# Kernel tuning notes

Hardware: AMD Instinct MI355X
Metric: run time of the kernel (lower is better)

Reference implementation:

```python
import jax, jax.numpy as jnp
import numpy as np

B = 4096          # effective_batch_size (world_size=1)
D = 128           # embedding_dim
T = 0.5           # temperature
CW = 0.5          # confidence_weight
PT = 0.8          # positive_threshold (cosine)


def setup_inputs() -> dict:
    key = jax.random.key(0)
    emb = jax.random.normal(key, (B, D), dtype=jnp.float32)
    emb = emb / jnp.linalg.norm(emb, axis=1, keepdims=True)  # cosine-sim embeddings
    return {"embedding": emb}


def reference(embedding):
    b = embedding.shape[0]
    half = b // 2
    idx = jnp.arange(b)
    pos_idx = (idx + half) % b  # positive pair index (other augmented view)

    # exp(sim / T), [B, B]
    sim = jnp.exp(embedding @ embedding.T / T)

    # precomputed masks (world_size=1, rank=0, num_pos=2):
    # positive mask: the other view; negative mask: everything except self and its pair
    pos_mask = jnp.zeros((b, b), dtype=sim.dtype).at[idx, pos_idx].set(1.0)
    neg_mask = 1.0 - pos_mask - jnp.eye(b, dtype=sim.dtype)

    all_pos = sim * pos_mask
    all_neg = sim * neg_mask

    pos_sim = sim[idx, pos_idx]  # [B]

    # diff_sim: |sim - pos_sim| on upper triangle (j >= i), 3 elsewhere,
    # with diagonal and (i, i+half) for i < half also set to 3
    upper = idx[None, :] >= idx[:, None]
    excl = jnp.eye(b, dtype=bool) | ((idx[:, None] < half) & (idx[None, :] == idx[:, None] + half))
    diff_sim = jnp.where(upper & ~excl, jnp.abs(sim - pos_sim[:, None]), jnp.asarray(3.0, sim.dtype))

    # all argmin locations (torch.where(diff_sim == min)) -> boolean select mask
    min_mask = diff_sim == jnp.min(diff_sim)
    conf = (jnp.log(pos_sim) * T >= PT)[:, None]  # per-anchor confidence gate
    sel = min_mask & conf

    # false-negative reweighting (pos read of all_neg happens before neg update)
    new_pos = jnp.where(sel & (all_pos == 0.0), CW * all_neg, all_pos)
    new_neg = jnp.where(sel & (all_neg != 0.0), (1.0 - CW) * all_neg, all_neg)

    pos = jnp.sum(new_pos, axis=1)
    neg = jnp.sum(new_neg, axis=1)
    return -jnp.mean(jnp.log(pos / (pos + neg)))
```

## Files before the change

### kernel.cpp

```cpp
#include <hip/hip_runtime.h>
#include <hip/hip_bf16.h>
#include <math.h>

#define B_N  4096
#define HALF 2048
#define D_K  128
#define TI   128
#define TJ   64
#define NTI  32
#define NTJ  64
#define JPB  4
#define NJG  (NTJ / JPB)

typedef __attribute__((ext_vector_type(8))) short bf16x8;
typedef __attribute__((ext_vector_type(4))) float f32x4;

__device__ __forceinline__ ushort f2bf(float x) {
    unsigned u = __float_as_uint(x);
    unsigned r = u + 0x7FFFu + ((u >> 16) & 1u);
    return (ushort)(r >> 16);
}

__device__ __forceinline__ void gload_lds16(const ushort* g, ushort* l) {
    __builtin_amdgcn_global_load_lds(
        (const __attribute__((address_space(1))) unsigned int*)g,
        (__attribute__((address_space(3))) unsigned int*)l, 16, 0, 0);
}

__device__ __forceinline__ bf16x8 read_fragB(const ushort* lds, int row, int kbyte) {
    int byte = ((row << 8) | kbyte) ^ ((row & 7) << 4);
    return *(const bf16x8*)((const char*)lds + byte);
}

__global__ __launch_bounds__(256) void k0_prep(const float* __restrict__ emb,
                                               ushort* __restrict__ embh,
                                               float* __restrict__ pos_sim,
                                               float* __restrict__ conf,
                                               float* __restrict__ neg_acc,
                                               unsigned* __restrict__ counter) {
    int gtid = blockIdx.x * 256 + threadIdx.x;
    float4 v = ((const float4*)emb)[gtid];
    float4 p = ((const float4*)emb)[gtid ^ 65536];
    ushort4 h;
    h.x = f2bf(v.x); h.y = f2bf(v.y); h.z = f2bf(v.z); h.w = f2bf(v.w);
    ((ushort4*)embh)[gtid] = h;
    float d = 0.f;
    d = fmaf(v.x, p.x, d); d = fmaf(v.y, p.y, d);
    d = fmaf(v.z, p.z, d); d = fmaf(v.w, p.w, d);
#pragma unroll
    for (int off = 1; off < 32; off <<= 1) d += __shfl_xor(d, off);
    if ((gtid & 31) == 0) {
        int r = gtid >> 5;
        float ps = expf(d * 2.0f);
        pos_sim[r] = ps;
        conf[r]    = (logf(ps) * 0.5f >= 0.8f) ? 1.0f : 0.0f;
        neg_acc[r] = 0.f;
    }
    if (gtid == 0) *counter = 0u;
}

__global__ __launch_bounds__(256, 3) void k1_main(const ushort* __restrict__ embh,
                                                  const float* __restrict__ pos_sim,
                                                  const float* __restrict__ conf,
                                                  float* __restrict__ neg_acc,
                                                  float* __restrict__ corrpart,
                                                  unsigned* __restrict__ tile_min) {
    int bi = blockIdx.y, jg = blockIdx.x;
    __shared__ ushort B0[TJ * D_K];
    __shared__ ushort B1[TJ * D_K];

    int tid = threadIdx.x, lane = tid & 63, wr = tid >> 6;
    int l15 = lane & 15;
    int k8  = (lane >> 4) << 3;
    int jr4 = (lane >> 4) << 2;

    {
        const ushort* srcB = embh + (size_t)(jg * JPB) * TJ * D_K;
#pragma unroll
        for (int it = 0; it < 4; ++it) {
            int f = tid + 256 * it;
            int r = f >> 4, c = f & 15;
            int g = (r << 4) | (c ^ (r & 7));
            gload_lds16(srcB + g * 8, B0 + f * 8);
        }
    }

    int I0 = bi * TI + wr * 32;
    bf16x8 A0[4], A1[4];
    {
        const ushort* a0 = embh + (size_t)(I0 + l15) * D_K + k8;
        const ushort* a1 = embh + (size_t)(I0 + 16 + l15) * D_K + k8;
#pragma unroll
        for (int ks = 0; ks < 4; ++ks) {
            A0[ks] = *(const bf16x8*)(a0 + ks * 32);
            A1[ks] = *(const bf16x8*)(a1 + ks * 32);
        }
    }

    int jtd = I0 >> 6;
    float psi0 = pos_sim[I0 + l15];
    float psi1 = pos_sim[I0 + 16 + l15];
    float cf0  = conf[I0 + l15];
    float cf1  = conf[I0 + 16 + l15];
    bool anyc  = __any((cf0 != 0.f) || (cf1 != 0.f));
    float negacc0 = 0.f, negacc1 = 0.f;
    float tl[JPB];

    __syncthreads();

#pragma unroll
    for (int t = 0; t < JPB; ++t) {
        const ushort* Bc = (t & 1) ? B1 : B0;
        ushort*       Bn = (t & 1) ? B0 : B1;
        int jt = jg * JPB + t;

        if (t + 1 < JPB) {
            const ushort* srcB = embh + (size_t)(jt + 1) * TJ * D_K;
#pragma unroll
            for (int it = 0; it < 4; ++it) {
                int f = tid + 256 * it;
                int r = f >> 4, c = f & 15;
                int g = (r << 4) | (c ^ (r & 7));
                gload_lds16(srcB + g * 8, Bn + f * 8);
            }
        }

        f32x4 acc[2][4];
#pragma unroll
        for (int m = 0; m < 2; ++m)
#pragma unroll
            for (int n = 0; n < 4; ++n) acc[m][n] = (f32x4){0.f, 0.f, 0.f, 0.f};
#pragma unroll
        for (int ks = 0; ks < 4; ++ks) {
            int kb = ks * 64 + (k8 << 1);
            bf16x8 b[4];
#pragma unroll
            for (int n = 0; n < 4; ++n) b[n] = read_fragB(Bc, l15 + n * 16, kb);
#pragma unroll
            for (int n = 0; n < 4; ++n) {
                acc[0][n] = __builtin_amdgcn_mfma_f32_16x16x32_bf16(b[n], A0[ks], acc[0][n], 0, 0, 0);
                acc[1][n] = __builtin_amdgcn_mfma_f32_16x16x32_bf16(b[n], A1[ks], acc[1][n], 0, 0, 0);
            }
        }
#pragma unroll
        for (int m = 0; m < 2; ++m)
#pragma unroll
            for (int n = 0; n < 4; ++n)
#pragma unroll
                for (int reg = 0; reg < 4; ++reg)
                    acc[m][n][reg] = __expf(acc[m][n][reg] * 2.0f);

        int j0 = jt * TJ;
        bool mixed = (jt == jtd), postt = (jt == (jtd ^ 32)), upT = (jt > jtd);
        float tmin = 3.0f;
#pragma unroll
        for (int m = 0; m < 2; ++m) {
            int i = I0 + m * 16 + l15;
            float psi = m ? psi1 : psi0;
            float np = 0.f;
            if (mixed) {
#pragma unroll
                for (int n = 0; n < 4; ++n)
#pragma unroll
                    for (int reg = 0; reg < 4; ++reg) {
                        float s = acc[m][n][reg];
                        int j = j0 + n * 16 + jr4 + reg;
                        if (j != i) np += s;
                        if (j > i)  tmin = fminf(tmin, fabsf(s - psi));
                    }
            } else if (postt) {
                int pidx = i ^ HALF;
#pragma unroll
                for (int n = 0; n < 4; ++n)
#pragma unroll
                    for (int reg = 0; reg < 4; ++reg) {
                        float s = acc[m][n][reg];
                        int j = j0 + n * 16 + jr4 + reg;
                        if (j != pidx) {
                            np += s;
                            if (upT) tmin = fminf(tmin, fabsf(s - psi));
                        }
                    }
            } else {
                float l0 = 3.f, l1 = 3.f, l2 = 3.f, l3 = 3.f;
#pragma unroll
                for (int n = 0; n < 4; ++n) {
                    float s0 = acc[m][n][0], s1 = acc[m][n][1];
                    float s2 = acc[m][n][2], s3 = acc[m][n][3];
                    np += (s0 + s1) + (s2 + s3);
                    if (upT) {
                        l0 = fminf(l0, fabsf(s0 - psi)); l1 = fminf(l1, fabsf(s1 - psi));
                        l2 = fminf(l2, fabsf(s2 - psi)); l3 = fminf(l3, fabsf(s3 - psi));
                    }
                }
                tmin = fminf(tmin, fminf(fminf(l0, l1), fminf(l2, l3)));
            }
            if (m) negacc1 += np; else negacc0 += np;
        }
        tl[t] = tmin;

        if (anyc) {
            float wt = tmin;
#pragma unroll
            for (int off = 32; off; off >>= 1)
                wt = fminf(wt, __shfl_xor(wt, off));
            tl[t] = wt;
#pragma unroll
            for (int m = 0; m < 2; ++m) {
                int i = I0 + m * 16 + l15;
                float psi = m ? psi1 : psi0;
                bool ci = ((m ? cf1 : cf0) != 0.f);
                float corr = 0.f;
#pragma unroll
                for (int n = 0; n < 4; ++n)
#pragma unroll
                    for (int reg = 0; reg < 4; ++reg) {
                        float s = acc[m][n][reg];
                        int j = j0 + n * 16 + jr4 + reg;
                        float d = 3.0f;
                        if (mixed)      { if (j > i) d = fabsf(s - psi); }
                        else if (postt) { if (upT && j != (i ^ HALF)) d = fabsf(s - psi); }
                        else if (upT)   d = fabsf(s - psi);
                        if (ci && d == wt) corr += 0.5f * s;
                    }
                corr += __shfl_xor(corr, 16);
                corr += __shfl_xor(corr, 32);
                if (lane < 16) corrpart[(size_t)jt * B_N + i] = corr;
            }
        }
        if (t + 1 < JPB) __syncthreads();
    }

#pragma unroll
    for (int off = 32; off; off >>= 1) {
#pragma unroll
        for (int t = 0; t < JPB; ++t)
            tl[t] = fminf(tl[t], __shfl_xor(tl[t], off));
    }
    if (lane == 0) {
        int base = (bi * 4 + wr) * NTJ + jg * JPB;
        tile_min[base + 0] = __float_as_uint(tl[0]);
        tile_min[base + 1] = __float_as_uint(tl[1]);
        tile_min[base + 2] = __float_as_uint(tl[2]);
        tile_min[base + 3] = __float_as_uint(tl[3]);
    }

    if (!anyc && lane < 16) {
#pragma unroll
        for (int t = 0; t < JPB; ++t) {
            corrpart[(size_t)(jg * JPB + t) * B_N + I0 + lane]      = 0.f;
            corrpart[(size_t)(jg * JPB + t) * B_N + I0 + 16 + lane] = 0.f;
        }
    }

    negacc0 += __shfl_xor(negacc0, 16);
    negacc0 += __shfl_xor(negacc0, 32);
    negacc1 += __shfl_xor(negacc1, 16);
    negacc1 += __shfl_xor(negacc1, 32);
    if (lane < 16) {
        atomicAdd(&neg_acc[I0 + lane],      negacc0);
        atomicAdd(&neg_acc[I0 + 16 + lane], negacc1);
    }
}

__global__ __launch_bounds__(128) void k3_loss(const float* __restrict__ pos_sim,
                                               const float* __restrict__ neg_acc,
                                               const float* __restrict__ corrpart,
                                               const unsigned* __restrict__ tile_min,
                                               float* __restrict__ partial,
                                               unsigned* __restrict__ counter,
                                               float* __restrict__ out) {
    int t = threadIdx.x, bi = blockIdx.x;
    unsigned gmv = 0xFFFFFFFFu;
#pragma unroll
    for (int k = 0; k < 64; ++k) gmv = min(gmv, tile_min[t + 128 * k]);
#pragma unroll
    for (int off = 32; off; off >>= 1) {
        unsigned o = (unsigned)__shfl_xor((int)gmv, off);
        gmv = min(gmv, o);
    }
    __shared__ unsigned gred[2];
    if ((t & 63) == 0) gred[t >> 6] = gmv;
    __syncthreads();
    unsigned gm = min(gred[0], gred[1]);

    int i = bi * 128 + t;
    int si = i >> 5;
    float corr = 0.f;
#pragma unroll 8
    for (int jt = 0; jt < NTJ; ++jt)
        if (tile_min[si * NTJ + jt] == gm)
            corr += corrpart[(size_t)jt * B_N + i];
    float pos = pos_sim[i] + corr;
    float neg = neg_acc[i] - corr;
    float l = logf(pos / (pos + neg));
#pragma unroll
    for (int off = 32; off; off >>= 1) l += __shfl_xor(l, off);
    __shared__ float w2[2];
    if ((t & 63) == 0) w2[t >> 6] = l;
    __syncthreads();
    if (t == 0) {
        partial[bi] = w2[0] + w2[1];
        __threadfence();
        unsigned c = atomicAdd(counter, 1u);
        if (c == NTI - 1) {
            __threadfence();
            float tot = 0.f;
            volatile float* vp = partial;
            for (int b = 0; b < NTI; ++b) tot += vp[b];
            *out = -tot / (float)B_N;
        }
    }
}

extern "C" void kernel_launch(void* const* d_in, const int* in_sizes, int n_in,
                              void* d_out, int out_size, void* d_ws, size_t ws_size,
                              hipStream_t stream) {
    const float* emb = (const float*)d_in[0];
    float* out = (float*)d_out;

    char* ws = (char*)d_ws;
    ushort*   embh      = (ushort*)ws;
    float*    fbase     = (float*)(ws + 1048576);
    float*    pos_sim   = fbase;
    float*    conf      = fbase + 4096;
    float*    neg_acc   = fbase + 8192;
    float*    corrpart  = fbase + 12288;
    float*    partial   = corrpart + (size_t)NTJ * B_N;
    unsigned* tile_min  = (unsigned*)(partial + 32);
    unsigned* counter   = tile_min + 128 * NTJ;

    k0_prep<<<512, 256, 0, stream>>>(emb, embh, pos_sim, conf, neg_acc, counter);
    k1_main<<<dim3(NJG, NTI), 256, 0, stream>>>(embh, pos_sim, conf, neg_acc,
                                                corrpart, tile_min);
    k3_loss<<<NTI, 128, 0, stream>>>(pos_sim, neg_acc, corrpart, tile_min,
                                     partial, counter, out);
}
```

Measured before the change: 32.62 us.

## Fuse loss reduction into main kernel via last-block-done tail

Removes the separate loss kernel. The last block of the main kernel, found with an atomic counter, now computes the global min, the corrections and the final mean. Per-row negative sums are written as 16 partial slices instead of atomically added, which also drops the zeroing in prep. The cost is that one block does the whole 4096-row tail serially, using a compacted list of min-matching tiles with a fallback path.

```diff
diff --git a/kernel.cpp b/kernel.cpp
--- a/kernel.cpp
+++ b/kernel.cpp
@@ -10,7 +10,8 @@
 #define NTI  32
 #define NTJ  64
 #define JPB  4
-#define NJG  (NTJ / JPB)
+#define NJG  16
+#define GRID 512
 
 typedef __attribute__((ext_vector_type(8))) short bf16x8;
 typedef __attribute__((ext_vector_type(4))) float f32x4;
@@ -36,8 +37,7 @@
                                                ushort* __restrict__ embh,
                                                float* __restrict__ pos_sim,
                                                float* __restrict__ conf,
-                                               float* __restrict__ neg_acc,
-                                               unsigned* __restrict__ counter) {
+                                               unsigned* __restrict__ fincnt) {
     int gtid = blockIdx.x * 256 + threadIdx.x;
     float4 v = ((const float4*)emb)[gtid];
     float4 p = ((const float4*)emb)[gtid ^ 65536];
@@ -54,25 +54,26 @@
         float ps = expf(d * 2.0f);
         pos_sim[r] = ps;
         conf[r]    = (logf(ps) * 0.5f >= 0.8f) ? 1.0f : 0.0f;
-        neg_acc[r] = 0.f;
-    }
-    if (gtid == 0) *counter = 0u;
+    }
+    if (gtid == 0) *fincnt = 0u;
 }
 
 __global__ __launch_bounds__(256, 3) void k1_main(const ushort* __restrict__ embh,
                                                   const float* __restrict__ pos_sim,
                                                   const float* __restrict__ conf,
-                                                  float* __restrict__ neg_acc,
+                                                  float* __restrict__ negpart,
                                                   float* __restrict__ corrpart,
-                                                  unsigned* __restrict__ tile_min) {
-    int bi = blockIdx.y, jg = blockIdx.x;
-    __shared__ ushort B0[TJ * D_K];
-    __shared__ ushort B1[TJ * D_K];
-
+                                                  unsigned* __restrict__ tile_min,
+                                                  unsigned* __restrict__ fincnt,
+                                                  float* __restrict__ out) {
     int tid = threadIdx.x, lane = tid & 63, wr = tid >> 6;
+    int bi = blockIdx.x >> 4, jg = blockIdx.x & 15;
     int l15 = lane & 15;
     int k8  = (lane >> 4) << 3;
     int jr4 = (lane >> 4) << 2;
+
+    __shared__ ushort B0[TJ * D_K];
+    __shared__ ushort B1[TJ * D_K];
 
     {
         const ushort* srcB = embh + (size_t)(jg * JPB) * TJ * D_K;
@@ -244,7 +245,6 @@
         tile_min[base + 2] = __float_as_uint(tl[2]);
         tile_min[base + 3] = __float_as_uint(tl[3]);
     }
-
     if (!anyc && lane < 16) {
 #pragma unroll
         for (int t = 0; t < JPB; ++t) {
@@ -252,65 +252,80 @@
             corrpart[(size_t)(jg * JPB + t) * B_N + I0 + 16 + lane] = 0.f;
         }
     }
-
     negacc0 += __shfl_xor(negacc0, 16);
     negacc0 += __shfl_xor(negacc0, 32);
     negacc1 += __shfl_xor(negacc1, 16);
     negacc1 += __shfl_xor(negacc1, 32);
     if (lane < 16) {
-        atomicAdd(&neg_acc[I0 + lane],      negacc0);
-        atomicAdd(&neg_acc[I0 + 16 + lane], negacc1);
-    }
-}
-
-__global__ __launch_bounds__(128) void k3_loss(const float* __restrict__ pos_sim,
-                                               const float* __restrict__ neg_acc,
-                                               const float* __restrict__ corrpart,
-                                               const unsigned* __restrict__ tile_min,
-                                               float* __restrict__ partial,
-                                               unsigned* __restrict__ counter,
-                                               float* __restrict__ out) {
-    int t = threadIdx.x, bi = blockIdx.x;
+        negpart[(size_t)jg * B_N + I0 + lane]      = negacc0;
+        negpart[(size_t)jg * B_N + I0 + 16 + lane] = negacc1;
+    }
+
+    __threadfence();
+    __syncthreads();
+    __shared__ unsigned rank;
+    if (tid == 0) rank = atomicAdd(fincnt, 1u);
+    __syncthreads();
+    if (rank != GRID - 1) return;
+    __threadfence();
+
+    __shared__ unsigned lcnt, gred[4], lslot[128];
+    __shared__ float w4[4];
+    if (tid == 0) lcnt = 0;
     unsigned gmv = 0xFFFFFFFFu;
 #pragma unroll
-    for (int k = 0; k < 64; ++k) gmv = min(gmv, tile_min[t + 128 * k]);
+    for (int k = 0; k < 32; ++k) gmv = min(gmv, tile_min[tid + 256 * k]);
 #pragma unroll
     for (int off = 32; off; off >>= 1) {
         unsigned o = (unsigned)__shfl_xor((int)gmv, off);
         gmv = min(gmv, o);
     }
-    __shared__ unsigned gred[2];
-    if ((t & 63) == 0) gred[t >> 6] = gmv;
-    __syncthreads();
-    unsigned gm = min(gred[0], gred[1]);
-
-    int i = bi * 128 + t;
-    int si = i >> 5;
-    float corr = 0.f;
-#pragma unroll 8
-    for (int jt = 0; jt < NTJ; ++jt)
-        if (tile_min[si * NTJ + jt] == gm)
-            corr += corrpart[(size_t)jt * B_N + i];
-    float pos = pos_sim[i] + corr;
-    float neg = neg_acc[i] - corr;
-    float l = logf(pos / (pos + neg));
-#pragma unroll
-    for (int off = 32; off; off >>= 1) l += __shfl_xor(l, off);
-    __shared__ float w2[2];
-    if ((t & 63) == 0) w2[t >> 6] = l;
-    __syncthreads();
-    if (t == 0) {
-        partial[bi] = w2[0] + w2[1];
-        __threadfence();
-        unsigned c = atomicAdd(counter, 1u);
-        if (c == NTI - 1) {
-            __threadfence();
-            float tot = 0.f;
-            volatile float* vp = partial;
-            for (int b = 0; b < NTI; ++b) tot += vp[b];
-            *out = -tot / (float)B_N;
-        }
-    }
+    if (lane == 0) gred[wr] = gmv;
+    __syncthreads();
+    unsigned gm = min(min(gred[0], gred[1]), min(gred[2], gred[3]));
+
+#pragma unroll
+    for (int k = 0; k < 32; ++k) {
+        int x = tid + 256 * k;
+        if (tile_min[x] == gm) {
+            unsigned p = atomicAdd(&lcnt, 1u);
+            if (p < 128) lslot[p] = (unsigned)x;
+        }
+    }
+    __syncthreads();
+    unsigned nl = lcnt;
+    bool fallback = (nl > 128u);
+    if (fallback) nl = 0;
+
+    float lsum = 0.f;
+#pragma unroll
+    for (int rr = 0; rr < 16; ++rr) {
+        int i = tid + rr * 256;
+        int si = i >> 5;
+        float nsum = 0.f;
+#pragma unroll
+        for (int p = 0; p < 16; ++p) nsum += negpart[(size_t)p * B_N + i];
+        float corr = 0.f;
+        if (!fallback) {
+            for (unsigned e = 0; e < nl; ++e) {
+                unsigned x = lslot[e];
+                if ((int)(x >> 6) == si) corr += corrpart[(size_t)(x & 63) * B_N + i];
+            }
+        } else {
+            for (int jt = 0; jt < NTJ; ++jt)
+                if (tile_min[si * NTJ + jt] == gm)
+                    corr += corrpart[(size_t)jt * B_N + i];
+        }
+        float pos = pos_sim[i] + corr;
+        float neg = nsum - corr;
+        lsum += logf(pos / (pos + neg));
+    }
+#pragma unroll
+    for (int off = 32; off; off >>= 1) lsum += __shfl_xor(lsum, off);
+    if (lane == 0) w4[wr] = lsum;
+    __syncthreads();
+    if (tid == 0)
+        *out = -((w4[0] + w4[1]) + (w4[2] + w4[3])) / (float)B_N;
 }
 
 extern "C" void kernel_launch(void* const* d_in, const int* in_sizes, int n_in,
@@ -320,19 +335,16 @@
     float* out = (float*)d_out;
 
     char* ws = (char*)d_ws;
-    ushort*   embh      = (ushort*)ws;
-    float*    fbase     = (float*)(ws + 1048576);
-    float*    pos_sim   = fbase;
-    float*    conf      = fbase + 4096;
-    float*    neg_acc   = fbase + 8192;
-    float*    corrpart  = fbase + 12288;
-    float*    partial   = corrpart + (size_t)NTJ * B_N;
-    unsigned* tile_min  = (unsigned*)(partial + 32);
-    unsigned* counter   = tile_min + 128 * NTJ;
-
-    k0_prep<<<512, 256, 0, stream>>>(emb, embh, pos_sim, conf, neg_acc, counter);
-    k1_main<<<dim3(NJG, NTI), 256, 0, stream>>>(embh, pos_sim, conf, neg_acc,
-                                                corrpart, tile_min);
-    k3_loss<<<NTI, 128, 0, stream>>>(pos_sim, neg_acc, corrpart, tile_min,
-                                     partial, counter, out);
-}
+    ushort*   embh     = (ushort*)ws;
+    float*    fbase    = (float*)(ws + (1 << 20));
+    float*    pos_sim  = fbase;
+    float*    conf     = fbase + 4096;
+    float*    negpart  = fbase + 8192;
+    float*    corrpart = negpart + 16 * B_N;
+    unsigned* tile_min = (unsigned*)(corrpart + (size_t)NTJ * B_N);
+    unsigned* fincnt   = tile_min + 128 * NTJ;
+
+    k0_prep<<<512, 256, 0, stream>>>(emb, embh, pos_sim, conf, fincnt);
+    k1_main<<<GRID, 256, 0, stream>>>(embh, pos_sim, conf, negpart, corrpart,
+                                      tile_min, fincnt, out);
+}
```

Measured after the change: 106.3 us. 3.26x slower.
